# Kernel tuning notes

Measured on AMD Instinct MI355X. Metric: run time of the kernel, lower is better.

Reference implementation:

```python
import jax, jax.numpy as jnp
import numpy as np

N = 50000      # nodes
E = 800000     # directed edges (self-loops added in reference)
F_IN = 64      # input features
HID = 64       # hidden channels
HEADS = 4
NCLS = 3
G = 64         # graphs in batch
EPS = 1e-5
NEG_SLOPE = 0.2


def setup_inputs() -> dict:
    key = jax.random.key(0)
    ks = jax.random.split(key, 20)
    s = 0.1
    inp = {
        "x": jax.random.normal(ks[0], (N, F_IN), jnp.float32),
        "edge_index": jax.random.randint(ks[1], (2, E), 0, N, jnp.int64),
        "batch": jnp.sort(jax.random.randint(ks[2], (N,), 0, G, jnp.int64)),
        # GATConv 1: F_IN -> HID per head, HEADS heads, concat
        "W1": jax.random.normal(ks[3], (F_IN, HEADS * HID), jnp.float32) * s,
        "a_src1": jax.random.normal(ks[4], (HEADS, HID), jnp.float32) * s,
        "a_dst1": jax.random.normal(ks[5], (HEADS, HID), jnp.float32) * s,
        "b1": jnp.zeros((HEADS * HID,), jnp.float32),
        # BatchNorm1d(256) eval-mode params
        "g1": jnp.ones((HEADS * HID,), jnp.float32),
        "be1": jnp.zeros((HEADS * HID,), jnp.float32),
        "m1": jnp.zeros((HEADS * HID,), jnp.float32),
        "v1": jnp.ones((HEADS * HID,), jnp.float32),
        # GATConv 2: 256 -> HID, 1 head
        "W2": jax.random.normal(ks[6], (HEADS * HID, HID), jnp.float32) * s,
        "a_src2": jax.random.normal(ks[7], (1, HID), jnp.float32) * s,
        "a_dst2": jax.random.normal(ks[8], (1, HID), jnp.float32) * s,
        "b2": jnp.zeros((HID,), jnp.float32),
        # BatchNorm1d(64)
        "g2": jnp.ones((HID,), jnp.float32),
        "be2": jnp.zeros((HID,), jnp.float32),
        "m2": jnp.zeros((HID,), jnp.float32),
        "v2": jnp.ones((HID,), jnp.float32),
        # MLP head
        "lw1": jax.random.normal(ks[9], (HID, HID // 2), jnp.float32) * s,
        "lb1": jnp.zeros((HID // 2,), jnp.float32),
        "lw2": jax.random.normal(ks[10], (HID // 2, NCLS), jnp.float32) * s,
        "lb2": jnp.zeros((NCLS,), jnp.float32),
    }
    return inp


def _gat(x, src, dst, W, a_s, a_d, b):
    """PyG-style GATConv: gather, LeakyReLU score, segment-softmax over dst, scatter-add."""
    H_, C_ = a_s.shape
    h = (x @ W).reshape(-1, H_, C_)                       # [N,H,C]
    es = jnp.einsum('nhc,hc->nh', h, a_s)                 # per-node src score
    ed = jnp.einsum('nhc,hc->nh', h, a_d)                 # per-node dst score
    e = jax.nn.leaky_relu(es[src] + ed[dst], NEG_SLOPE)   # [Etot,H]
    m = jax.ops.segment_max(e, dst, num_segments=N)       # stable softmax per dst
    p = jnp.exp(e - m[dst])
    denom = jax.ops.segment_sum(p, dst, num_segments=N)
    alpha = p / denom[dst]                                # [Etot,H]
    out = jax.ops.segment_sum(h[src] * alpha[:, :, None], dst, num_segments=N)
    return out.reshape(-1, H_ * C_) + b


def _bn(x, g, b, mean, var):
    return (x - mean) * jax.lax.rsqrt(var + EPS) * g + b


def reference(x, W1, a_src1, a_dst1, b1, g1, be1, m1, v1,
              W2, a_src2, a_dst2, b2, g2, be2, m2, v2,
              lw1, lb1, lw2, lb2, edge_index, batch):
    loop = jnp.arange(N, dtype=edge_index.dtype)
    src = jnp.concatenate([edge_index[0], loop])          # add self-loops
    dst = jnp.concatenate([edge_index[1], loop])
    h = _gat(x, src, dst, W1, a_src1, a_dst1, b1)
    h = jax.nn.elu(_bn(h, g1, be1, m1, v1))
    h = _gat(h, src, dst, W2, a_src2, a_dst2, b2)
    h = _bn(h, g2, be2, m2, v2)
    # global_mean_pool over graphs
    sums = jax.ops.segment_sum(h, batch, num_segments=G)
    cnt = jax.ops.segment_sum(jnp.ones((N, 1), h.dtype), batch, num_segments=G)
    pooled = sums / jnp.maximum(cnt, 1.0)                 # [G, HID]
    z = jax.nn.relu(pooled @ lw1 + lb1)
    z = z @ lw2 + lb2
    return jax.nn.log_softmax(z, axis=1)
```

## Files before the change

kernel.cpp:

```cpp
#include <hip/hip_runtime.h>
#include <math.h>

#define N_NODES 50000
#define N_EDGES 800000
#define ETOT    (N_EDGES + N_NODES)
#define GGRAPHS 64
#define EPS_BN  1e-5f

typedef __attribute__((ext_vector_type(8))) short short8;
typedef __attribute__((ext_vector_type(4))) float f32x4;
typedef __attribute__((ext_vector_type(2))) float f32x2;

__device__ __forceinline__ unsigned short f2bf(float f) {
    union { float f; unsigned u; } v; v.f = f;
    unsigned r = v.u + 0x7fffu + ((v.u >> 16) & 1u);
    return (unsigned short)(r >> 16);
}
__device__ __forceinline__ float leaky(float e) {
    return fmaxf(e, 0.2f * e);
}
__device__ __forceinline__ unsigned pack4_fp8(float a, float b, float c, float d) {
    int v = __builtin_amdgcn_cvt_pk_fp8_f32(a, b, 0, false);
    v = __builtin_amdgcn_cvt_pk_fp8_f32(c, d, v, true);
    return (unsigned)v;
}
__device__ __forceinline__ short8 cvt8(const float* p) {
    float4 u = *(const float4*)p;
    float4 v = *(const float4*)(p + 4);
    short8 r;
    r[0] = (short)f2bf(u.x); r[1] = (short)f2bf(u.y);
    r[2] = (short)f2bf(u.z); r[3] = (short)f2bf(u.w);
    r[4] = (short)f2bf(v.x); r[5] = (short)f2bf(v.y);
    r[6] = (short)f2bf(v.z); r[7] = (short)f2bf(v.w);
    return r;
}

#define NBUK 196
#define EPB  4096
#define NBLK2 ((ETOT + EPB - 1) / EPB)
#define CAPR 6144


#define PREP2_T (32768 + 320)
#define NPREP ((PREP2_T + 255) / 256)

__global__ __launch_bounds__(256)
void k_prepfill(const float* __restrict__ W1, const float* __restrict__ W2,
                const float* __restrict__ b1, const float* __restrict__ g1,
                const float* __restrict__ be1, const float* __restrict__ m1,
                const float* __restrict__ v1,
                const float* __restrict__ b2, const float* __restrict__ g2,
                const float* __restrict__ be2, const float* __restrict__ m2,
                const float* __restrict__ v2,
                const int* __restrict__ ei,
                unsigned short* __restrict__ W1T,
                unsigned short* __restrict__ W2T,
                float* __restrict__ A1s, float* __restrict__ B1s,
                float* __restrict__ A2s, float* __restrict__ B2s,
                int* __restrict__ gcur, unsigned* __restrict__ pairs) {
    __shared__ int lcnt[NBUK];
    __shared__ int lbase[NBUK];
    if (blockIdx.x < NPREP) {
        int t = blockIdx.x * 256 + threadIdx.x;
        if (t < 16384) {
            int i = t;
            int n = i >> 6, k = i & 63;
            W1T[i] = f2bf(W1[k * 256 + n]);
        } else if (t < 32768) {
            int i = t - 16384;
            int n = i >> 8, kp = i & 255;
            int rk = (kp & 15) * 16 + (kp >> 4);
            W2T[i] = f2bf(W2[rk * 64 + n]);
        } else if (t < 32768 + 256) {
            int z = t - 32768;
            int r = (z & 15) * 16 + (z >> 4);
            float A = g1[r] * rsqrtf(v1[r] + EPS_BN);
            A1s[z] = A;
            B1s[z] = (b1[r] - m1[r]) * A + be1[r];
        } else if (t < PREP2_T) {
            int z = t - 32768 - 256;
            int r = (z & 3) * 16 + (z >> 2);
            float A = g2[r] * rsqrtf(v2[r] + EPS_BN);
            A2s[z] = A;
            B2s[z] = (b2[r] - m2[r]) * A + be2[r];
        }
        return;
    }
    int t = threadIdx.x;
    int blk = blockIdx.x - NPREP;
    for (int i = t; i < NBUK; i += 256) lcnt[i] = 0;
    __syncthreads();
    int e0 = blk * EPB;
    int ds[16], ss[16];
#pragma unroll
    for (int j = 0; j < 16; ++j) {
        int e = e0 + j * 256 + t;
        int s = -1, d = -1;
        if (e < ETOT) {
            if (e < N_EDGES) { s = ei[e]; d = ei[N_EDGES + e]; }
            else             { s = d = e - N_EDGES; }
            atomicAdd(&lcnt[d >> 8], 1);
        }
        ds[j] = d; ss[j] = s;
    }
    __syncthreads();
    for (int i = t; i < NBUK; i += 256) {
        int c = lcnt[i];
        lbase[i] = i * CAPR + (c ? atomicAdd(&gcur[i], c) : 0);
    }
    __syncthreads();
#pragma unroll
    for (int j = 0; j < 16; ++j) {
        if (ds[j] >= 0) {
            int bk = ds[j] >> 8;
            int pos = atomicAdd(&lbase[bk], 1);
            if (pos < (bk + 1) * CAPR)
                pairs[pos] = (unsigned)ss[j] | ((unsigned)(ds[j] & 255) << 16);
        }
    }
}


__global__ __launch_bounds__(256)
void k_bsum(const int* __restrict__ gcur, int* __restrict__ bstart,
            int* __restrict__ offs) {
    __shared__ int s[256];
    int t = threadIdx.x;
    int v = (t < NBUK) ? gcur[t] : 0;
    s[t] = v; __syncthreads();
    for (int d2 = 1; d2 < 256; d2 <<= 1) {
        int add = (t >= d2) ? s[t - d2] : 0;
        __syncthreads();
        s[t] += add;
        __syncthreads();
    }
    if (t < NBUK) bstart[t] = s[t] - v;
    if (t == 0) { bstart[NBUK] = ETOT; offs[N_NODES] = ETOT; }
}


#define CAP 6144

__global__ __launch_bounds__(256)
void k_csr(const unsigned* __restrict__ pairs, const int* __restrict__ gcur,
           const int* __restrict__ bstart, int* __restrict__ offs,
           unsigned short* __restrict__ csr) {
    __shared__ unsigned sp[CAP];
    __shared__ unsigned short lc[CAP];
    __shared__ int c256[256];
    __shared__ int o256[256];
    __shared__ int s[256];
    int b = blockIdx.x, t = threadIdx.x;
    int base = bstart[b];
    int n = gcur[b];
    int node = b * 256 + t;
    const unsigned* reg = pairs + (size_t)b * CAPR;
    for (int i = t; i < n; i += 256) sp[i] = reg[i];
    c256[t] = 0;
    __syncthreads();
    for (int i = t; i < n; i += 256) atomicAdd(&c256[(sp[i] >> 16) & 255], 1);
    __syncthreads();
    int v = c256[t];
    s[t] = v; __syncthreads();
    for (int d2 = 1; d2 < 256; d2 <<= 1) {
        int add = (t >= d2) ? s[t - d2] : 0;
        __syncthreads();
        s[t] += add;
        __syncthreads();
    }
    int myoff = s[t] - v;
    o256[t] = myoff;
    if (node < N_NODES) offs[node] = base + myoff;
    __syncthreads();
    for (int i = t; i < n; i += 256) {
        unsigned p = sp[i];
        int pos = atomicAdd(&o256[(p >> 16) & 255], 1);
        lc[pos] = (unsigned short)(p & 0xffff);
    }
    __syncthreads();
    for (int i = t; i < n; i += 256) csr[base + i] = lc[i];
}


__global__ __launch_bounds__(256)
void k_gemm1(const float* __restrict__ x, const unsigned short* __restrict__ W1Tg,
             const float* __restrict__ a_s, const float* __restrict__ a_d,
             unsigned char* __restrict__ h1f8, float* __restrict__ es1, float* __restrict__ ed1) {
    __shared__ unsigned short W1T[256 * 72];
    int t = threadIdx.x;
    for (int c = t; c < 2048; c += 256) {
        int n = c >> 3, k8 = (c & 7) * 8;
        *(short8*)&W1T[n * 72 + k8] = *(const short8*)&W1Tg[n * 64 + k8];
    }
    __syncthreads();
    int wid = t >> 6, lane = t & 63;
    int quad = lane >> 4, col = lane & 15;
    float as_r[16], ad_r[16];
#pragma unroll
    for (int i = 0; i < 16; ++i) {
        as_r[i] = a_s[i * 16 + col];
        ad_r[i] = a_d[i * 16 + col];
    }
    int tile = blockIdx.x * 4 + wid;
    if (tile >= 3125) return;
    int base = tile * 16;
    short8 a0 = cvt8(&x[(size_t)(base + col) * 64 + quad * 8]);
    short8 a1 = cvt8(&x[(size_t)(base + col) * 64 + 32 + quad * 8]);
    f32x4 acc[16];
#pragma unroll
    for (int nt = 0; nt < 16; ++nt) acc[nt] = (f32x4){0.f, 0.f, 0.f, 0.f};
#pragma unroll
    for (int nt = 0; nt < 16; ++nt) {
        short8 b0 = *(const short8*)&W1T[(nt * 16 + col) * 72 + quad * 8];
        short8 b1 = *(const short8*)&W1T[(nt * 16 + col) * 72 + 32 + quad * 8];
        acc[nt] = __builtin_amdgcn_mfma_f32_16x16x32_bf16(a0, b0, acc[nt], 0, 0, 0);
        acc[nt] = __builtin_amdgcn_mfma_f32_16x16x32_bf16(a1, b1, acc[nt], 0, 0, 0);
    }
    float esp[16], edp[16];
#pragma unroll
    for (int i = 0; i < 16; ++i) { esp[i] = 0.f; edp[i] = 0.f; }
#pragma unroll
    for (int nt = 0; nt < 16; ++nt) {
        int hd = nt >> 2;
#pragma unroll
        for (int r = 0; r < 4; ++r) {
            esp[hd * 4 + r] += acc[nt][r] * as_r[nt];
            edp[hd * 4 + r] += acc[nt][r] * ad_r[nt];
        }
    }
#pragma unroll
    for (int i = 0; i < 16; ++i) {
        float v = esp[i], w = edp[i];
#pragma unroll
        for (int m = 1; m <= 8; m <<= 1) { v += __shfl_xor(v, m); w += __shfl_xor(w, m); }
        esp[i] = v; edp[i] = w;
    }
    if (col == 0) {
#pragma unroll
        for (int hd = 0; hd < 4; ++hd)
#pragma unroll
            for (int r = 0; r < 4; ++r) {
                int node = base + quad * 4 + r;
                es1[node * 4 + hd] = esp[hd * 4 + r];
                ed1[node * 4 + hd] = edp[hd * 4 + r];
            }
    }
#pragma unroll
    for (int r = 0; r < 4; ++r) {
        uint4 pk;
        pk.x = pack4_fp8(acc[0][r],  acc[1][r],  acc[2][r],  acc[3][r]);
        pk.y = pack4_fp8(acc[4][r],  acc[5][r],  acc[6][r],  acc[7][r]);
        pk.z = pack4_fp8(acc[8][r],  acc[9][r],  acc[10][r], acc[11][r]);
        pk.w = pack4_fp8(acc[12][r], acc[13][r], acc[14][r], acc[15][r]);
        *(uint4*)&h1f8[(size_t)(base + quad * 4 + r) * 256 + col * 16] = pk;
    }
}


__global__ __launch_bounds__(256)
void k_gat1g2(const unsigned char* __restrict__ h1f8, const float* __restrict__ es1,
              const float* __restrict__ ed1, const int* __restrict__ offs,
              const unsigned short* __restrict__ csr,
              const float* __restrict__ A1s, const float* __restrict__ B1s,
              const unsigned short* __restrict__ W2Tg,
              const float* __restrict__ a_s2, const float* __restrict__ a_d2,
              unsigned char* __restrict__ h2f8, float* __restrict__ es2,
              float* __restrict__ ed2) {
    __shared__ unsigned short hbt[16][264];
    __shared__ float esps[4][16], edps[4][16];
    __shared__ uint4 h2t4[64];
    unsigned char* h2t = (unsigned char*)h2t4;
    int tid = threadIdx.x;
    int l = tid & 63;
    int gbase = l & 48;
    int q = tid & 15;
    int dl = tid >> 4;
    int nbase = blockIdx.x * 16;
    int d = nbase + dl;
    int start = offs[d], deg = offs[d + 1] - start;
    int e4 = q >> 2, hd = q & 3;
    float edv = ed1[d * 4 + hd];
    const unsigned char* hrow = h1f8 + q * 16;
    float a[16];
#pragma unroll
    for (int i = 0; i < 16; ++i) a[i] = 0.f;
    float wsum = 0.f;
    for (int c0 = 0; c0 < deg; c0 += 4) {
        int idx = c0 + e4;
        int s = csr[start + min(idx, deg - 1)];
        float w = (idx < deg) ? __expf(leaky(es1[s * 4 + hd] + edv)) : 0.f;
        wsum += w;
        int se[4];
#pragma unroll
        for (int e = 0; e < 4; ++e) se[e] = __shfl(s, gbase | (e << 2));
        uint4 rv[4];
#pragma unroll
        for (int e = 0; e < 4; ++e)
            rv[e] = *(const uint4*)(hrow + ((size_t)(unsigned)se[e] << 8));
#pragma unroll
        for (int e = 0; e < 4; ++e) {
            float w0 = __shfl(w, gbase | (e << 2) | 0);
            float w1 = __shfl(w, gbase | (e << 2) | 1);
            float w2 = __shfl(w, gbase | (e << 2) | 2);
            float w3 = __shfl(w, gbase | (e << 2) | 3);
            f32x2 p;
            p = __builtin_amdgcn_cvt_pk_f32_fp8((int)rv[e].x, false); a[0]  += w0 * p.x; a[1]  += w0 * p.y;
            p = __builtin_amdgcn_cvt_pk_f32_fp8((int)rv[e].x, true);  a[2]  += w0 * p.x; a[3]  += w0 * p.y;
            p = __builtin_amdgcn_cvt_pk_f32_fp8((int)rv[e].y, false); a[4]  += w1 * p.x; a[5]  += w1 * p.y;
            p = __builtin_amdgcn_cvt_pk_f32_fp8((int)rv[e].y, true);  a[6]  += w1 * p.x; a[7]  += w1 * p.y;
            p = __builtin_amdgcn_cvt_pk_f32_fp8((int)rv[e].z, false); a[8]  += w2 * p.x; a[9]  += w2 * p.y;
            p = __builtin_amdgcn_cvt_pk_f32_fp8((int)rv[e].z, true);  a[10] += w2 * p.x; a[11] += w2 * p.y;
            p = __builtin_amdgcn_cvt_pk_f32_fp8((int)rv[e].w, false); a[12] += w3 * p.x; a[13] += w3 * p.y;
            p = __builtin_amdgcn_cvt_pk_f32_fp8((int)rv[e].w, true);  a[14] += w3 * p.x; a[15] += w3 * p.y;
        }
    }
    wsum += __shfl_xor(wsum, 4);
    wsum += __shfl_xor(wsum, 8);
    float inv[4];
#pragma unroll
    for (int h = 0; h < 4; ++h) inv[h] = 1.f / __shfl(wsum, gbase | h);
#pragma unroll
    for (int i0 = 0; i0 < 4; ++i0) {
        float4 Av = *(const float4*)&A1s[q * 16 + i0 * 4];
        float4 Bv = *(const float4*)&B1s[q * 16 + i0 * 4];
        float o0 = a[i0 * 4 + 0] * inv[i0] * Av.x + Bv.x;
        float o1 = a[i0 * 4 + 1] * inv[i0] * Av.y + Bv.y;
        float o2 = a[i0 * 4 + 2] * inv[i0] * Av.z + Bv.z;
        float o3 = a[i0 * 4 + 3] * inv[i0] * Av.w + Bv.w;
        o0 = (o0 > 0.f) ? o0 : expm1f(o0);
        o1 = (o1 > 0.f) ? o1 : expm1f(o1);
        o2 = (o2 > 0.f) ? o2 : expm1f(o2);
        o3 = (o3 > 0.f) ? o3 : expm1f(o3);
        ushort4 ov;
        ov.x = f2bf(o0); ov.y = f2bf(o1); ov.z = f2bf(o2); ov.w = f2bf(o3);
        *(ushort4*)&hbt[dl][q * 16 + i0 * 4] = ov;
    }
    __syncthreads();
    int w = tid >> 6;
    int quad = l >> 4, col = l & 15;
    short8 af[8];
#pragma unroll
    for (int kk = 0; kk < 8; ++kk)
        af[kk] = *(const short8*)&hbt[col][kk * 32 + quad * 8];
    f32x4 acc = (f32x4){0.f, 0.f, 0.f, 0.f};
#pragma unroll
    for (int kk = 0; kk < 8; ++kk) {
        short8 b = *(const short8*)&W2Tg[(w * 16 + col) * 256 + kk * 32 + quad * 8];
        acc = __builtin_amdgcn_mfma_f32_16x16x32_bf16(af[kk], b, acc, 0, 0, 0);
    }
    float asw = a_s2[w * 16 + col], adw = a_d2[w * 16 + col];
    float esp[4], edp[4];
#pragma unroll
    for (int r = 0; r < 4; ++r) { esp[r] = acc[r] * asw; edp[r] = acc[r] * adw; }
#pragma unroll
    for (int r = 0; r < 4; ++r) {
#pragma unroll
        for (int m = 1; m <= 8; m <<= 1) {
            esp[r] += __shfl_xor(esp[r], m);
            edp[r] += __shfl_xor(edp[r], m);
        }
    }
    if (col == 0) {
#pragma unroll
        for (int r = 0; r < 4; ++r) {
            esps[w][quad * 4 + r] = esp[r];
            edps[w][quad * 4 + r] = edp[r];
        }
    }
#pragma unroll
    for (int r = 0; r < 4; ++r) {
        unsigned pk = pack4_fp8(acc[r], acc[r], acc[r], acc[r]);
        h2t[(quad * 4 + r) * 64 + col * 4 + w] = (unsigned char)(pk & 0xff);
    }
    __syncthreads();
    if (tid < 16) {
        es2[nbase + tid] = esps[0][tid] + esps[1][tid] + esps[2][tid] + esps[3][tid];
        ed2[nbase + tid] = edps[0][tid] + edps[1][tid] + edps[2][tid] + edps[3][tid];
    }
    if (tid < 64) {
        int node = tid >> 2, c = tid & 3;
        *(uint4*)&h2f8[(size_t)(nbase + node) * 64 + c * 16] = h2t4[node * 4 + c];
    }
}


__global__ __launch_bounds__(256)
void k_gat2p(const unsigned char* __restrict__ h2f8, const float* __restrict__ es2,
             const float* __restrict__ ed2, const int* __restrict__ offs,
             const unsigned short* __restrict__ csr,
             const float* __restrict__ A2s, const float* __restrict__ B2s,
             const int* __restrict__ batch, float* __restrict__ pooled) {
    __shared__ float ot[16][68];
    __shared__ int gbat[16];
    int tid = threadIdx.x;
    int l = tid & 63;
    int gbase = l & 48;
    int q = tid & 15;
    int dl = tid >> 4;
    int nbase = blockIdx.x * 16;
    int d = nbase + dl;
    int start = offs[d], deg = offs[d + 1] - start;
    float edv = ed2[d];
    const unsigned char* hrow = h2f8 + q * 4;
    float a0 = 0.f, a1 = 0.f, a2 = 0.f, a3 = 0.f, wsum = 0.f;
    int e4 = q & 3;
    for (int c0 = 0; c0 < deg; c0 += 4) {
        int idx = c0 + e4;
        int s = csr[start + min(idx, deg - 1)];
        float w = (idx < deg) ? __expf(leaky(es2[s] + edv)) : 0.f;
        wsum += w;
        int se[4];
#pragma unroll
        for (int e = 0; e < 4; ++e) se[e] = __shfl(s, gbase | e);
        unsigned rv[4];
#pragma unroll
        for (int e = 0; e < 4; ++e)
            rv[e] = *(const unsigned*)(hrow + ((size_t)(unsigned)se[e] << 6));
#pragma unroll
        for (int e = 0; e < 4; ++e) {
            float we = __shfl(w, gbase | e);
            f32x2 p;
            p = __builtin_amdgcn_cvt_pk_f32_fp8((int)rv[e], false); a0 += we * p.x; a1 += we * p.y;
            p = __builtin_amdgcn_cvt_pk_f32_fp8((int)rv[e], true);  a2 += we * p.x; a3 += we * p.y;
        }
    }
    wsum += __shfl_xor(wsum, 1);
    wsum += __shfl_xor(wsum, 2);
    float inv = 1.f / wsum;
    float4 Av = *(const float4*)&A2s[q * 4];
    float4 Bv = *(const float4*)&B2s[q * 4];
    ot[dl][q * 4 + 0] = a0 * inv * Av.x + Bv.x;
    ot[dl][q * 4 + 1] = a1 * inv * Av.y + Bv.y;
    ot[dl][q * 4 + 2] = a2 * inv * Av.z + Bv.z;
    ot[dl][q * 4 + 3] = a3 * inv * Av.w + Bv.w;
    if (tid < 16) gbat[tid] = batch[nbase + tid];
    __syncthreads();
    if (tid < 64) {
        int ch = tid;
        int curg = gbat[0];
        float acc = 0.f;
#pragma unroll
        for (int n = 0; n < 16; ++n) {
            int g = gbat[n];
            if (g != curg) {
                atomicAdd(&pooled[curg * 64 + ch], acc);
                acc = 0.f;
                curg = g;
            }
            acc += ot[n][ch];
        }
        atomicAdd(&pooled[curg * 64 + ch], acc);
    }
}


__device__ int lower_bound_i(const int* a, int n, int key) {
    int lo = 0, hi = n;
    while (lo < hi) {
        int mid = (lo + hi) >> 1;
        if (a[mid] < key) lo = mid + 1; else hi = mid;
    }
    return lo;
}

__global__ void k_head(const float* __restrict__ pooled, const int* __restrict__ batch,
                       const float* __restrict__ lw1, const float* __restrict__ lb1,
                       const float* __restrict__ lw2, const float* __restrict__ lb2,
                       float* __restrict__ out) {
    int g = threadIdx.x;
    if (g >= GGRAPHS) return;
    int s0 = lower_bound_i(batch, N_NODES, g);
    int s1 = lower_bound_i(batch, N_NODES, g + 1);
    int cnt = s1 - s0;
    float invc = 1.f / (float)((cnt > 0) ? cnt : 1);
    float p[64];
#pragma unroll
    for (int c = 0; c < 64; ++c) p[c] = pooled[g * 64 + c] * invc;
    float z0 = lb2[0], z1 = lb2[1], z2 = lb2[2];
    for (int j = 0; j < 32; ++j) {
        float hj = lb1[j];
#pragma unroll
        for (int c = 0; c < 64; ++c) {
            int rc = (c & 3) * 16 + (c >> 2);
            hj += p[c] * lw1[rc * 32 + j];
        }
        hj = fmaxf(hj, 0.f);
        z0 += hj * lw2[j * 3 + 0];
        z1 += hj * lw2[j * 3 + 1];
        z2 += hj * lw2[j * 3 + 2];
    }
    float m = fmaxf(z0, fmaxf(z1, z2));
    float lse = logf(expf(z0 - m) + expf(z1 - m) + expf(z2 - m)) + m;
    out[g * 3 + 0] = z0 - lse;
    out[g * 3 + 1] = z1 - lse;
    out[g * 3 + 2] = z2 - lse;
}


extern "C" void kernel_launch(void* const* d_in, const int* in_sizes, int n_in,
                              void* d_out, int out_size, void* d_ws, size_t ws_size,
                              hipStream_t stream) {
    (void)in_sizes; (void)n_in; (void)out_size; (void)ws_size;
    const float* x    = (const float*)d_in[0];
    const int*   ei   = (const int*)d_in[1];
    const int*   batch= (const int*)d_in[2];
    const float* W1   = (const float*)d_in[3];
    const float* a_s1 = (const float*)d_in[4];
    const float* a_d1 = (const float*)d_in[5];
    const float* b1   = (const float*)d_in[6];
    const float* g1   = (const float*)d_in[7];
    const float* be1  = (const float*)d_in[8];
    const float* m1   = (const float*)d_in[9];
    const float* v1   = (const float*)d_in[10];
    const float* W2   = (const float*)d_in[11];
    const float* a_s2 = (const float*)d_in[12];
    const float* a_d2 = (const float*)d_in[13];
    const float* b2   = (const float*)d_in[14];
    const float* g2   = (const float*)d_in[15];
    const float* be2  = (const float*)d_in[16];
    const float* m2   = (const float*)d_in[17];
    const float* v2   = (const float*)d_in[18];
    const float* lw1  = (const float*)d_in[19];
    const float* lb1  = (const float*)d_in[20];
    const float* lw2  = (const float*)d_in[21];
    const float* lb2  = (const float*)d_in[22];
    float* out = (float*)d_out;

    char* ws = (char*)d_ws;
    size_t off = 0;
    auto alloc = [&](size_t bytes) -> void* {
        void* p = ws + off;
        off += (bytes + 255) & ~(size_t)255;
        return p;
    };
    float* pooled = (float*)alloc((size_t)GGRAPHS * 64 * 4);
    int*   gcur   = (int*)alloc((size_t)NBUK * 4);
    unsigned short* W1T = (unsigned short*)alloc((size_t)16384 * 2);
    unsigned short* W2T = (unsigned short*)alloc((size_t)16384 * 2);
    unsigned char*  h1  = (unsigned char*)alloc((size_t)N_NODES * 256);
    unsigned char*  h2  = (unsigned char*)alloc((size_t)N_NODES * 64);
    float* es1  = (float*)alloc((size_t)N_NODES * 4 * 4);
    float* ed1  = (float*)alloc((size_t)N_NODES * 4 * 4);
    float* es2  = (float*)alloc((size_t)N_NODES * 4);
    float* ed2  = (float*)alloc((size_t)N_NODES * 4);
    float* A1s  = (float*)alloc(256 * 4);
    float* B1s  = (float*)alloc(256 * 4);
    float* A2s  = (float*)alloc(64 * 4);
    float* B2s  = (float*)alloc(64 * 4);
    int*   offs = (int*)alloc((size_t)(N_NODES + 1) * 4);
    unsigned short* csr = (unsigned short*)alloc((size_t)ETOT * 2);
    unsigned* pairs = (unsigned*)alloc((size_t)NBUK * CAPR * 4);
    int* bstart = (int*)alloc((size_t)(NBUK + 1) * 4);

    const int ntileb = (3125 + 3) / 4;
    const int ngat = 3125;

    hipMemsetAsync(pooled, 0, 16384 + 1024, stream);
    k_prepfill<<<NPREP + NBLK2, 256, 0, stream>>>(W1, W2, b1, g1, be1, m1, v1,
                                                  b2, g2, be2, m2, v2, ei,
                                                  W1T, W2T, A1s, B1s, A2s, B2s,
                                                  gcur, pairs);
    k_bsum<<<1, 256, 0, stream>>>(gcur, bstart, offs);
    k_csr<<<NBUK, 256, 0, stream>>>(pairs, gcur, bstart, offs, csr);

    k_gemm1<<<ntileb, 256, 0, stream>>>(x, W1T, a_s1, a_d1, h1, es1, ed1);
    k_gat1g2<<<ngat, 256, 0, stream>>>(h1, es1, ed1, offs, csr, A1s, B1s,
                                       W2T, a_s2, a_d2, h2, es2, ed2);
    k_gat2p<<<ngat, 256, 0, stream>>>(h2, es2, ed2, offs, csr, A2s, B2s,
                                      batch, pooled);
    k_head<<<1, 64, 0, stream>>>(pooled, batch, lw1, lb1, lw2, lb2, out);
}
```

Measured before the change: 236.4 us.

## Fuse edge bucketing, weight prep and first GEMM into one kernel launch

Merges the edge-bucketing pass, the W2/BN parameter prep and the layer-1 GEMM into one launch with block-range dispatch. Each GEMM block now transposes and converts W1 to bf16 into shared memory itself, instead of reading a prebuilt W1T. The bucket prefix-sum kernel is folded into the CSR kernel, where every block recomputes the 196-entry scan. Separately, the layer-2 aggregation processes 8 edges per iteration instead of 4. The goal is fewer launches and more independent work running concurrently, at the cost of redundant per-block W1 conversion with strided global reads.

```diff
diff --git a/kernel.cpp b/kernel.cpp
--- a/kernel.cpp
+++ b/kernel.cpp
@@ -24,61 +24,88 @@
     v = __builtin_amdgcn_cvt_pk_fp8_f32(c, d, v, true);
     return (unsigned)v;
 }
-__device__ __forceinline__ short8 cvt8(const float* p) {
-    float4 u = *(const float4*)p;
-    float4 v = *(const float4*)(p + 4);
-    short8 r;
-    r[0] = (short)f2bf(u.x); r[1] = (short)f2bf(u.y);
-    r[2] = (short)f2bf(u.z); r[3] = (short)f2bf(u.w);
-    r[4] = (short)f2bf(v.x); r[5] = (short)f2bf(v.y);
-    r[6] = (short)f2bf(v.z); r[7] = (short)f2bf(v.w);
-    return r;
-}
 
 #define NBUK 196
 #define EPB  4096
 #define NBLK2 ((ETOT + EPB - 1) / EPB)
 #define CAPR 6144
-
-
-#define PREP2_T (32768 + 320)
-#define NPREP ((PREP2_T + 255) / 256)
+#define CAP  6144
+
+#define PREPW_T (16384 + 320)
+#define NPREPW ((PREPW_T + 255) / 256)
+#define NT1B 782
+#define NMEGA (NBLK2 + NPREPW + NT1B)
+
 
 __global__ __launch_bounds__(256)
-void k_prepfill(const float* __restrict__ W1, const float* __restrict__ W2,
-                const float* __restrict__ b1, const float* __restrict__ g1,
-                const float* __restrict__ be1, const float* __restrict__ m1,
-                const float* __restrict__ v1,
-                const float* __restrict__ b2, const float* __restrict__ g2,
-                const float* __restrict__ be2, const float* __restrict__ m2,
-                const float* __restrict__ v2,
-                const int* __restrict__ ei,
-                unsigned short* __restrict__ W1T,
-                unsigned short* __restrict__ W2T,
-                float* __restrict__ A1s, float* __restrict__ B1s,
-                float* __restrict__ A2s, float* __restrict__ B2s,
-                int* __restrict__ gcur, unsigned* __restrict__ pairs) {
+void k_mega(const float* __restrict__ x, const int* __restrict__ ei,
+            const float* __restrict__ W1, const float* __restrict__ W2,
+            const float* __restrict__ b1, const float* __restrict__ g1,
+            const float* __restrict__ be1, const float* __restrict__ m1,
+            const float* __restrict__ v1,
+            const float* __restrict__ b2, const float* __restrict__ g2,
+            const float* __restrict__ be2, const float* __restrict__ m2,
+            const float* __restrict__ v2,
+            const float* __restrict__ a_s, const float* __restrict__ a_d,
+            unsigned short* __restrict__ W2T,
+            float* __restrict__ A1s, float* __restrict__ B1s,
+            float* __restrict__ A2s, float* __restrict__ B2s,
+            int* __restrict__ gcur, unsigned* __restrict__ pairs,
+            unsigned char* __restrict__ h1f8,
+            float* __restrict__ es1, float* __restrict__ ed1) {
+    __shared__ unsigned short W1T[256 * 72];
     __shared__ int lcnt[NBUK];
     __shared__ int lbase[NBUK];
-    if (blockIdx.x < NPREP) {
-        int t = blockIdx.x * 256 + threadIdx.x;
-        if (t < 16384) {
-            int i = t;
-            int n = i >> 6, k = i & 63;
-            W1T[i] = f2bf(W1[k * 256 + n]);
-        } else if (t < 32768) {
-            int i = t - 16384;
-            int n = i >> 8, kp = i & 255;
+    int t = threadIdx.x;
+    int b = blockIdx.x;
+
+    if (b < NBLK2) {
+        for (int i = t; i < NBUK; i += 256) lcnt[i] = 0;
+        __syncthreads();
+        int e0 = b * EPB;
+        int ds[16], ss[16];
+#pragma unroll
+        for (int j = 0; j < 16; ++j) {
+            int e = e0 + j * 256 + t;
+            int s = -1, d = -1;
+            if (e < ETOT) {
+                if (e < N_EDGES) { s = ei[e]; d = ei[N_EDGES + e]; }
+                else             { s = d = e - N_EDGES; }
+                atomicAdd(&lcnt[d >> 8], 1);
+            }
+            ds[j] = d; ss[j] = s;
+        }
+        __syncthreads();
+        for (int i = t; i < NBUK; i += 256) {
+            int c = lcnt[i];
+            lbase[i] = i * CAPR + (c ? atomicAdd(&gcur[i], c) : 0);
+        }
+        __syncthreads();
+#pragma unroll
+        for (int j = 0; j < 16; ++j) {
+            if (ds[j] >= 0) {
+                int bk = ds[j] >> 8;
+                int pos = atomicAdd(&lbase[bk], 1);
+                if (pos < (bk + 1) * CAPR)
+                    pairs[pos] = (unsigned)ss[j] | ((unsigned)(ds[j] & 255) << 16);
+            }
+        }
+        return;
+    }
+    if (b < NBLK2 + NPREPW) {
+        int t2 = (b - NBLK2) * 256 + t;
+        if (t2 < 16384) {
+            int n = t2 >> 8, kp = t2 & 255;
             int rk = (kp & 15) * 16 + (kp >> 4);
-            W2T[i] = f2bf(W2[rk * 64 + n]);
-        } else if (t < 32768 + 256) {
-            int z = t - 32768;
+            W2T[t2] = f2bf(W2[rk * 64 + n]);
+        } else if (t2 < 16384 + 256) {
+            int z = t2 - 16384;
             int r = (z & 15) * 16 + (z >> 4);
             float A = g1[r] * rsqrtf(v1[r] + EPS_BN);
             A1s[z] = A;
             B1s[z] = (b1[r] - m1[r]) * A + be1[r];
-        } else if (t < PREP2_T) {
-            int z = t - 32768 - 256;
+        } else if (t2 < PREPW_T) {
+            int z = t2 - 16384 - 256;
             int r = (z & 3) * 16 + (z >> 2);
             float A = g2[r] * rsqrtf(v2[r] + EPS_BN);
             A2s[z] = A;
@@ -86,112 +113,8 @@
         }
         return;
     }
-    int t = threadIdx.x;
-    int blk = blockIdx.x - NPREP;
-    for (int i = t; i < NBUK; i += 256) lcnt[i] = 0;
-    __syncthreads();
-    int e0 = blk * EPB;
-    int ds[16], ss[16];
-#pragma unroll
-    for (int j = 0; j < 16; ++j) {
-        int e = e0 + j * 256 + t;
-        int s = -1, d = -1;
-        if (e < ETOT) {
-            if (e < N_EDGES) { s = ei[e]; d = ei[N_EDGES + e]; }
-            else             { s = d = e - N_EDGES; }
-            atomicAdd(&lcnt[d >> 8], 1);
-        }
-        ds[j] = d; ss[j] = s;
-    }
-    __syncthreads();
-    for (int i = t; i < NBUK; i += 256) {
-        int c = lcnt[i];
-        lbase[i] = i * CAPR + (c ? atomicAdd(&gcur[i], c) : 0);
-    }
-    __syncthreads();
-#pragma unroll
-    for (int j = 0; j < 16; ++j) {
-        if (ds[j] >= 0) {
-            int bk = ds[j] >> 8;
-            int pos = atomicAdd(&lbase[bk], 1);
-            if (pos < (bk + 1) * CAPR)
-                pairs[pos] = (unsigned)ss[j] | ((unsigned)(ds[j] & 255) << 16);
-        }
-    }
-}
-
-
-__global__ __launch_bounds__(256)
-void k_bsum(const int* __restrict__ gcur, int* __restrict__ bstart,
-            int* __restrict__ offs) {
-    __shared__ int s[256];
-    int t = threadIdx.x;
-    int v = (t < NBUK) ? gcur[t] : 0;
-    s[t] = v; __syncthreads();
-    for (int d2 = 1; d2 < 256; d2 <<= 1) {
-        int add = (t >= d2) ? s[t - d2] : 0;
-        __syncthreads();
-        s[t] += add;
-        __syncthreads();
-    }
-    if (t < NBUK) bstart[t] = s[t] - v;
-    if (t == 0) { bstart[NBUK] = ETOT; offs[N_NODES] = ETOT; }
-}
-
-
-#define CAP 6144
-
-__global__ __launch_bounds__(256)
-void k_csr(const unsigned* __restrict__ pairs, const int* __restrict__ gcur,
-           const int* __restrict__ bstart, int* __restrict__ offs,
-           unsigned short* __restrict__ csr) {
-    __shared__ unsigned sp[CAP];
-    __shared__ unsigned short lc[CAP];
-    __shared__ int c256[256];
-    __shared__ int o256[256];
-    __shared__ int s[256];
-    int b = blockIdx.x, t = threadIdx.x;
-    int base = bstart[b];
-    int n = gcur[b];
-    int node = b * 256 + t;
-    const unsigned* reg = pairs + (size_t)b * CAPR;
-    for (int i = t; i < n; i += 256) sp[i] = reg[i];
-    c256[t] = 0;
-    __syncthreads();
-    for (int i = t; i < n; i += 256) atomicAdd(&c256[(sp[i] >> 16) & 255], 1);
-    __syncthreads();
-    int v = c256[t];
-    s[t] = v; __syncthreads();
-    for (int d2 = 1; d2 < 256; d2 <<= 1) {
-        int add = (t >= d2) ? s[t - d2] : 0;
-        __syncthreads();
-        s[t] += add;
-        __syncthreads();
-    }
-    int myoff = s[t] - v;
-    o256[t] = myoff;
-    if (node < N_NODES) offs[node] = base + myoff;
-    __syncthreads();
-    for (int i = t; i < n; i += 256) {
-        unsigned p = sp[i];
-        int pos = atomicAdd(&o256[(p >> 16) & 255], 1);
-        lc[pos] = (unsigned short)(p & 0xffff);
-    }
-    __syncthreads();
-    for (int i = t; i < n; i += 256) csr[base + i] = lc[i];
-}
-
-
-__global__ __launch_bounds__(256)
-void k_gemm1(const float* __restrict__ x, const unsigned short* __restrict__ W1Tg,
-             const float* __restrict__ a_s, const float* __restrict__ a_d,
-             unsigned char* __restrict__ h1f8, float* __restrict__ es1, float* __restrict__ ed1) {
-    __shared__ unsigned short W1T[256 * 72];
-    int t = threadIdx.x;
-    for (int c = t; c < 2048; c += 256) {
-        int n = c >> 3, k8 = (c & 7) * 8;
-        *(short8*)&W1T[n * 72 + k8] = *(const short8*)&W1Tg[n * 64 + k8];
-    }
+    for (int k = 0; k < 64; ++k)
+        W1T[t * 72 + k] = f2bf(W1[k * 256 + t]);
     __syncthreads();
     int wid = t >> 6, lane = t & 63;
     int quad = lane >> 4, col = lane & 15;
@@ -201,11 +124,23 @@
         as_r[i] = a_s[i * 16 + col];
         ad_r[i] = a_d[i * 16 + col];
     }
-    int tile = blockIdx.x * 4 + wid;
+    int tile = (b - NBLK2 - NPREPW) * 4 + wid;
     if (tile >= 3125) return;
     int base = tile * 16;
-    short8 a0 = cvt8(&x[(size_t)(base + col) * 64 + quad * 8]);
-    short8 a1 = cvt8(&x[(size_t)(base + col) * 64 + 32 + quad * 8]);
+    const float* xr = &x[(size_t)(base + col) * 64 + quad * 8];
+    float4 u0 = *(const float4*)xr;
+    float4 u1 = *(const float4*)(xr + 4);
+    float4 u2 = *(const float4*)(xr + 32);
+    float4 u3 = *(const float4*)(xr + 36);
+    short8 a0, a1;
+    a0[0] = (short)f2bf(u0.x); a0[1] = (short)f2bf(u0.y);
+    a0[2] = (short)f2bf(u0.z); a0[3] = (short)f2bf(u0.w);
+    a0[4] = (short)f2bf(u1.x); a0[5] = (short)f2bf(u1.y);
+    a0[6] = (short)f2bf(u1.z); a0[7] = (short)f2bf(u1.w);
+    a1[0] = (short)f2bf(u2.x); a1[1] = (short)f2bf(u2.y);
+    a1[2] = (short)f2bf(u2.z); a1[3] = (short)f2bf(u2.w);
+    a1[4] = (short)f2bf(u3.x); a1[5] = (short)f2bf(u3.y);
+    a1[6] = (short)f2bf(u3.z); a1[7] = (short)f2bf(u3.w);
     f32x4 acc[16];
 #pragma unroll
     for (int nt = 0; nt < 16; ++nt) acc[nt] = (f32x4){0.f, 0.f, 0.f, 0.f};
@@ -254,6 +189,58 @@
         pk.w = pack4_fp8(acc[12][r], acc[13][r], acc[14][r], acc[15][r]);
         *(uint4*)&h1f8[(size_t)(base + quad * 4 + r) * 256 + col * 16] = pk;
     }
+}
+
+
+__global__ __launch_bounds__(256)
+void k_csr(const unsigned* __restrict__ pairs, const int* __restrict__ gcur,
+           int* __restrict__ offs, unsigned short* __restrict__ csr) {
+    __shared__ unsigned sp[CAP];
+    __shared__ unsigned short lc[CAP];
+    __shared__ int c256[256];
+    __shared__ int o256[256];
+    __shared__ int s[256];
+    int b = blockIdx.x, t = threadIdx.x;
+    int v = (t < NBUK) ? gcur[t] : 0;
+    s[t] = v; __syncthreads();
+    for (int d2 = 1; d2 < 256; d2 <<= 1) {
+        int add = (t >= d2) ? s[t - d2] : 0;
+        __syncthreads();
+        s[t] += add;
+        __syncthreads();
+    }
+    int gb = gcur[b];
+    int base = s[b] - gb;
+    int total = s[NBUK - 1];
+    if (b == NBUK - 1 && t == 0) offs[N_NODES] = total;
+    __syncthreads();
+    int n = min(gb, CAP);
+    int node = b * 256 + t;
+    const unsigned* reg = pairs + (size_t)b * CAPR;
+    for (int i = t; i < n; i += 256) sp[i] = reg[i];
+    c256[t] = 0;
+    __syncthreads();
+    for (int i = t; i < n; i += 256) atomicAdd(&c256[(sp[i] >> 16) & 255], 1);
+    __syncthreads();
+    int v2 = c256[t];
+    s[t] = v2; __syncthreads();
+    for (int d2 = 1; d2 < 256; d2 <<= 1) {
+        int add = (t >= d2) ? s[t - d2] : 0;
+        __syncthreads();
+        s[t] += add;
+        __syncthreads();
+    }
+    int myoff = s[t] - v2;
+    o256[t] = myoff;
+    if (node < N_NODES) offs[node] = base + myoff;
+    __syncthreads();
+    for (int i = t; i < n; i += 256) {
+        unsigned p = sp[i];
+        int pos = atomicAdd(&o256[(p >> 16) & 255], 1);
+        lc[pos] = (unsigned short)(p & 0xffff);
+    }
+    __syncthreads();
+    for (int i = t; i < n; i += 256) csr[base + i] = lc[i];
 }
 
 
@@ -403,21 +390,21 @@
     float edv = ed2[d];
     const unsigned char* hrow = h2f8 + q * 4;
     float a0 = 0.f, a1 = 0.f, a2 = 0.f, a3 = 0.f, wsum = 0.f;
-    int e4 = q & 3;
-    for (int c0 = 0; c0 < deg; c0 += 4) {
-        int idx = c0 + e4;
+    int e8 = q & 7;
+    for (int c0 = 0; c0 < deg; c0 += 8) {
+        int idx = c0 + e8;
         int s = csr[start + min(idx, deg - 1)];
         float w = (idx < deg) ? __expf(leaky(es2[s] + edv)) : 0.f;
         wsum += w;
-        int se[4];
-#pragma unroll
-        for (int e = 0; e < 4; ++e) se[e] = __shfl(s, gbase | e);
-        unsigned rv[4];
-#pragma unroll
-        for (int e = 0; e < 4; ++e)
+        int se[8];
+#pragma unroll
+        for (int e = 0; e < 8; ++e) se[e] = __shfl(s, gbase | e);
+        unsigned rv[8];
+#pragma unroll
+        for (int e = 0; e < 8; ++e)
             rv[e] = *(const unsigned*)(hrow + ((size_t)(unsigned)se[e] << 6));
 #pragma unroll
-        for (int e = 0; e < 4; ++e) {
+        for (int e = 0; e < 8; ++e) {
             float we = __shfl(w, gbase | e);
             f32x2 p;
             p = __builtin_amdgcn_cvt_pk_f32_fp8((int)rv[e], false); a0 += we * p.x; a1 += we * p.y;
@@ -426,6 +413,7 @@
     }
     wsum += __shfl_xor(wsum, 1);
     wsum += __shfl_xor(wsum, 2);
+    wsum += __shfl_xor(wsum, 4);
     float inv = 1.f / wsum;
     float4 Av = *(const float4*)&A2s[q * 4];
     float4 Bv = *(const float4*)&B2s[q * 4];
@@ -535,7 +523,6 @@
     };
     float* pooled = (float*)alloc((size_t)GGRAPHS * 64 * 4);
     int*   gcur   = (int*)alloc((size_t)NBUK * 4);
-    unsigned short* W1T = (unsigned short*)alloc((size_t)16384 * 2);
     unsigned short* W2T = (unsigned short*)alloc((size_t)16384 * 2);
     unsigned char*  h1  = (unsigned char*)alloc((size_t)N_NODES * 256);
     unsigned char*  h2  = (unsigned char*)alloc((size_t)N_NODES * 64);
@@ -550,20 +537,17 @@
     int*   offs = (int*)alloc((size_t)(N_NODES + 1) * 4);
     unsigned short* csr = (unsigned short*)alloc((size_t)ETOT * 2);
     unsigned* pairs = (unsigned*)alloc((size_t)NBUK * CAPR * 4);
-    int* bstart = (int*)alloc((size_t)(NBUK + 1) * 4);
-
-    const int ntileb = (3125 + 3) / 4;
+
     const int ngat = 3125;
 
     hipMemsetAsync(pooled, 0, 16384 + 1024, stream);
-    k_prepfill<<<NPREP + NBLK2, 256, 0, stream>>>(W1, W2, b1, g1, be1, m1, v1,
-                                                  b2, g2, be2, m2, v2, ei,
-                                                  W1T, W2T, A1s, B1s, A2s, B2s,
-                                                  gcur, pairs);
-    k_bsum<<<1, 256, 0, stream>>>(gcur, bstart, offs);
-    k_csr<<<NBUK, 256, 0, stream>>>(pairs, gcur, bstart, offs, csr);
-
-    k_gemm1<<<ntileb, 256, 0, stream>>>(x, W1T, a_s1, a_d1, h1, es1, ed1);
+    k_mega<<<NMEGA, 256, 0, stream>>>(x, ei, W1, W2,
+                                      b1, g1, be1, m1, v1,
+                                      b2, g2, be2, m2, v2,
+                                      a_s1, a_d1,
+                                      W2T, A1s, B1s, A2s, B2s,
+                                      gcur, pairs, h1, es1, ed1);
+    k_csr<<<NBUK, 256, 0, stream>>>(pairs, gcur, offs, csr);
     k_gat1g2<<<ngat, 256, 0, stream>>>(h1, es1, ed1, offs, csr, A1s, B1s,
                                        W2T, a_s2, a_d2, h2, es2, ed2);
     k_gat2p<<<ngat, 256, 0, stream>>>(h2, es2, ed2, offs, csr, A2s, B2s,
```

Result: faster. 226.4 us (-4.2%).
